# Kernel optimization log

Measured on AMD Instinct MI355X. Metric: run time of the kernel, lower is better.

## Reference

```python
import jax, jax.numpy as jnp
import numpy as np

N_NODES = 100000
N_EDGES = 1600000
IN_CH = 128
HID = 256
OUT_CH = 128
N_GRAPHS = 2048


def setup_inputs() -> dict:
    key = jax.random.key(0)
    ks = jax.random.split(key, 12)
    x = jax.random.normal(ks[0], (N_NODES, IN_CH), dtype=jnp.float32)
    edge_index = jax.random.randint(ks[1], (2, N_EDGES), 0, N_NODES, dtype=jnp.int32)
    batch = jnp.sort(jax.random.randint(ks[2], (N_NODES,), 0, N_GRAPHS, dtype=jnp.int32))
    s = lambda k, shp, fan: jax.random.normal(k, shp, dtype=jnp.float32) / np.sqrt(fan)
    params = {
        # SAGEConv1: lin_l (applied to aggregated neighbors, has bias) and lin_r (root)
        "W1l": s(ks[3], (IN_CH, HID), IN_CH), "b1": jnp.zeros((HID,), jnp.float32),
        "W1r": s(ks[4], (IN_CH, HID), IN_CH),
        # SAGEConv2
        "W2l": s(ks[5], (HID, HID), HID), "b2": jnp.zeros((HID,), jnp.float32),
        "W2r": s(ks[6], (HID, HID), HID),
        # MLP head
        "W3": s(ks[7], (HID, HID), HID), "b3": jnp.zeros((HID,), jnp.float32),
        "W4": s(ks[8], (HID, OUT_CH), HID), "b4": jnp.zeros((OUT_CH,), jnp.float32),
    }
    return {"x": x, "edge_index": edge_index, "batch": batch, **params}


def _sage_conv(x, src, dst, Wl, bl, Wr, num_nodes):
    # PyG SAGEConv (aggr='mean'): out_i = Wl @ mean_{j->i} x_j + bl + Wr @ x_i
    agg = jax.ops.segment_sum(x[src], dst, num_segments=num_nodes)  # [N, C]
    cnt = jax.ops.segment_sum(jnp.ones((src.shape[0],), x.dtype), dst, num_segments=num_nodes)
    mean = agg / jnp.maximum(cnt, 1.0)[:, None]
    return mean @ Wl + bl + x @ Wr


def reference(x, edge_index, batch, W1l, b1, W1r, W2l, b2, W2r, W3, b3, W4, b4):
    src, dst = edge_index[0], edge_index[1]
    h = jax.nn.relu(_sage_conv(x, src, dst, W1l, b1, W1r, N_NODES))
    # dropout is identity in eval mode
    h = jax.nn.relu(_sage_conv(h, src, dst, W2l, b2, W2r, N_NODES))
    # global_mean_pool over graphs
    psum = jax.ops.segment_sum(h, batch, num_segments=N_GRAPHS)  # [G, HID]
    gcnt = jax.ops.segment_sum(jnp.ones((h.shape[0],), h.dtype), batch, num_segments=N_GRAPHS)
    pooled = psum / jnp.maximum(gcnt, 1.0)[:, None]
    # MLP head
    hidden = jax.nn.relu(pooled @ W3 + b3)
    return hidden @ W4 + b4  # [G, OUT_CH]
```

## Files before the change

### kernel.cpp

```cpp
#include <hip/hip_runtime.h>

#define N_NODES 100000
#define N_EDGES 1600000
#define IN_CH 128
#define HID 256
#define OUT_CH 128
#define N_GRAPHS 2048

#define NBUK 391
#define CHUNK 8192

typedef __attribute__((ext_vector_type(8))) short bf16x8;
typedef __attribute__((ext_vector_type(4))) float f32x4;
typedef __attribute__((ext_vector_type(2))) float f32x2;

__device__ inline unsigned short f2b(float f) {
    unsigned int u = __builtin_bit_cast(unsigned int, f);
    u = (u + 0x7FFF + ((u >> 16) & 1)) >> 16;
    return (unsigned short)u;
}
__device__ inline float b2f(unsigned short h) {
    unsigned int u = (unsigned int)h << 16;
    return __builtin_bit_cast(float, u);
}

#define GLOAD_LDS16(gsrc, ldst)                                                   \
    __builtin_amdgcn_global_load_lds(                                             \
        (const __attribute__((address_space(1))) void*)(gsrc),                    \
        (__attribute__((address_space(3))) void*)(ldst), 16, 0, 0)

#define SCAN_ITEMS 8
#define SCAN_TILE (256 * SCAN_ITEMS)

__global__ void scan1_k(const int* __restrict__ in, int* __restrict__ out,
                        int* __restrict__ bsums, int n) {
    __shared__ int wsum[4];
    int base = blockIdx.x * SCAN_TILE + (int)threadIdx.x * SCAN_ITEMS;
    int v[SCAN_ITEMS];
    int s = 0;
    #pragma unroll
    for (int i = 0; i < SCAN_ITEMS; ++i) {
        v[i] = (base + i < n) ? in[base + i] : 0;
        s += v[i];
    }
    int lane = threadIdx.x & 63, wid = threadIdx.x >> 6;
    int incl = s;
    #pragma unroll
    for (int off = 1; off < 64; off <<= 1) {
        int t = __shfl_up(incl, off, 64);
        if (lane >= off) incl += t;
    }
    if (lane == 63) wsum[wid] = incl;
    __syncthreads();
    int wprefix = 0;
    #pragma unroll
    for (int w = 0; w < 4; ++w)
        if (w < wid) wprefix += wsum[w];
    int run = wprefix + incl - s;
    #pragma unroll
    for (int i = 0; i < SCAN_ITEMS; ++i) {
        if (base + i < n) out[base + i] = run;
        run += v[i];
    }
    if (threadIdx.x == 255) bsums[blockIdx.x] = wprefix + incl;
}

__global__ void scan2_k(int* __restrict__ bsums, int nb, int* __restrict__ total) {
    __shared__ int wsum[4];
    int v = ((int)threadIdx.x < nb) ? bsums[threadIdx.x] : 0;
    int lane = threadIdx.x & 63, wid = threadIdx.x >> 6;
    int incl = v;
    #pragma unroll
    for (int off = 1; off < 64; off <<= 1) {
        int t = __shfl_up(incl, off, 64);
        if (lane >= off) incl += t;
    }
    if (lane == 63) wsum[wid] = incl;
    __syncthreads();
    int wprefix = 0;
    #pragma unroll
    for (int w = 0; w < 4; ++w)
        if (w < wid) wprefix += wsum[w];
    if ((int)threadIdx.x < nb) bsums[threadIdx.x] = wprefix + incl - v;
    if (threadIdx.x == 255) *total = wprefix + incl;
}

__global__ void bucket_count_k(const int* __restrict__ dst, int* __restrict__ bcnt, int E) {
    __shared__ int cnt[NBUK];
    int tid = threadIdx.x;
    for (int i = tid; i < NBUK; i += 256) cnt[i] = 0;
    __syncthreads();
    int e0 = blockIdx.x * CHUNK;
    int eend = min(e0 + CHUNK, E);
    for (int e = e0 + tid; e < eend; e += 256)
        atomicAdd(&cnt[dst[e] >> 8], 1);
    __syncthreads();
    for (int i = tid; i < NBUK; i += 256)
        if (cnt[i]) atomicAdd(&bcnt[i], cnt[i]);
}

__global__ void bin_scatter_k(const int* __restrict__ src, const int* __restrict__ dst,
                              const int* __restrict__ bbase, int* __restrict__ bcur,
                              uint2* __restrict__ staging, int E) {
    __shared__ int cnt[NBUK];
    __shared__ int gbase[NBUK];
    int tid = threadIdx.x;
    for (int i = tid; i < NBUK; i += 256) cnt[i] = 0;
    __syncthreads();
    int e0 = blockIdx.x * CHUNK;
    int eend = min(e0 + CHUNK, E);
    for (int e = e0 + tid; e < eend; e += 256)
        atomicAdd(&cnt[dst[e] >> 8], 1);
    __syncthreads();
    for (int i = tid; i < NBUK; i += 256) {
        int c = cnt[i];
        gbase[i] = c ? (bbase[i] + atomicAdd(&bcur[i], c)) : 0;
        cnt[i] = 0;
    }
    __syncthreads();
    for (int e = e0 + tid; e < eend; e += 256) {
        int d = dst[e];
        int b = d >> 8;
        int l = atomicAdd(&cnt[b], 1);
        uint2 p; p.x = (unsigned)src[e]; p.y = (unsigned)d;
        staging[(size_t)gbase[b] + l] = p;
    }
}

__global__ void csr_build_k(const uint2* __restrict__ staging, const int* __restrict__ bbase,
                            int* __restrict__ row_ofs, int* __restrict__ csr) {
    __shared__ int ldeg[256];
    __shared__ int lofs[256];
    __shared__ int wsum[4];
    int b = blockIdx.x, tid = threadIdx.x;
    int base = bbase[b];
    int cnt = bbase[b + 1] - base;
    ldeg[tid] = 0;
    __syncthreads();
    const uint2* sp = staging + base;
    for (int i = tid; i < cnt; i += 256)
        atomicAdd(&ldeg[sp[i].y & 255], 1);
    __syncthreads();
    int v = ldeg[tid];
    int lane = tid & 63, wid = tid >> 6;
    int incl = v;
    #pragma unroll
    for (int off = 1; off < 64; off <<= 1) {
        int t = __shfl_up(incl, off, 64);
        if (lane >= off) incl += t;
    }
    if (lane == 63) wsum[wid] = incl;
    __syncthreads();
    int wprefix = 0;
    #pragma unroll
    for (int w = 0; w < 4; ++w)
        if (w < wid) wprefix += wsum[w];
    int excl = wprefix + incl - v;
    lofs[tid] = excl;
    int node = b * 256 + tid;
    if (node < N_NODES) row_ofs[node] = base + excl;
    if (b == NBUK - 1 && tid == 0) row_ofs[N_NODES] = N_EDGES;
    ldeg[tid] = 0;
    __syncthreads();
    for (int i = tid; i < cnt; i += 256) {
        uint2 p = sp[i];
        int d = (int)p.y & 255;
        int pos = atomicAdd(&ldeg[d], 1);
        csr[base + lofs[d] + pos] = (int)p.x;
    }
}

__global__ void gofs_search_k(const int* __restrict__ batch, int* __restrict__ gofs,
                              int n, int G) {
    int g = blockIdx.x * blockDim.x + threadIdx.x;
    if (g > G) return;
    if (g == G) { gofs[G] = n; return; }
    int lo = 0, hi = n;
    while (lo < hi) {
        int mid = (lo + hi) >> 1;
        if (batch[mid] < g) lo = mid + 1; else hi = mid;
    }
    gofs[g] = lo;
}

__global__ void wt_concat_k(const float* __restrict__ Wl, const float* __restrict__ Wr,
                            unsigned short* __restrict__ out, int K1, int K2, int N) {
    int idx = blockIdx.x * blockDim.x + threadIdx.x;
    int KT = K1 + K2;
    if (idx >= N * KT) return;
    int n = idx / KT, k = idx % KT;
    float v = (k < K1) ? Wl[(size_t)k * N + n] : Wr[(size_t)(k - K1) * N + n];
    out[idx] = f2b(v);
}

__global__ void f2b8_k(const float* __restrict__ in, unsigned short* __restrict__ outb,
                       unsigned char* __restrict__ out8, size_t n8) {
    size_t i = (size_t)blockIdx.x * blockDim.x + threadIdx.x;
    if (i >= n8) return;
    float4 a = ((const float4*)in)[i * 2];
    float4 b = ((const float4*)in)[i * 2 + 1];
    unsigned short ob[8];
    ob[0] = f2b(a.x); ob[1] = f2b(a.y); ob[2] = f2b(a.z); ob[3] = f2b(a.w);
    ob[4] = f2b(b.x); ob[5] = f2b(b.y); ob[6] = f2b(b.z); ob[7] = f2b(b.w);
    ((uint4*)outb)[i] = *(const uint4*)ob;
    int w0 = 0, w1 = 0;
    w0 = __builtin_amdgcn_cvt_pk_fp8_f32(a.x, a.y, w0, false);
    w0 = __builtin_amdgcn_cvt_pk_fp8_f32(a.z, a.w, w0, true);
    w1 = __builtin_amdgcn_cvt_pk_fp8_f32(b.x, b.y, w1, false);
    w1 = __builtin_amdgcn_cvt_pk_fp8_f32(b.z, b.w, w1, true);
    uint2 o8; o8.x = (unsigned int)w0; o8.y = (unsigned int)w1;
    ((uint2*)out8)[i] = o8;
}

__global__ void b2f8_k(const unsigned short* __restrict__ in, unsigned char* __restrict__ out,
                       size_t n16) {
    size_t i = (size_t)blockIdx.x * blockDim.x + threadIdx.x;
    if (i >= n16) return;
    uint4 v0 = ((const uint4*)in)[i * 2];
    uint4 v1 = ((const uint4*)in)[i * 2 + 1];
    const unsigned int* q = (const unsigned int*)&v0;
    const unsigned int* r = (const unsigned int*)&v1;
    uint4 o;
    unsigned int* po = (unsigned int*)&o;
    #pragma unroll
    for (int t = 0; t < 2; ++t) {
        int w = 0;
        w = __builtin_amdgcn_cvt_pk_fp8_f32(b2f((unsigned short)(q[t * 2] & 0xFFFF)),
                                            b2f((unsigned short)(q[t * 2] >> 16)), w, false);
        w = __builtin_amdgcn_cvt_pk_fp8_f32(b2f((unsigned short)(q[t * 2 + 1] & 0xFFFF)),
                                            b2f((unsigned short)(q[t * 2 + 1] >> 16)), w, true);
        po[t] = (unsigned int)w;
    }
    #pragma unroll
    for (int t = 0; t < 2; ++t) {
        int w = 0;
        w = __builtin_amdgcn_cvt_pk_fp8_f32(b2f((unsigned short)(r[t * 2] & 0xFFFF)),
                                            b2f((unsigned short)(r[t * 2] >> 16)), w, false);
        w = __builtin_amdgcn_cvt_pk_fp8_f32(b2f((unsigned short)(r[t * 2 + 1] & 0xFFFF)),
                                            b2f((unsigned short)(r[t * 2 + 1] >> 16)), w, true);
        po[2 + t] = (unsigned int)w;
    }
    ((uint4*)out)[i] = o;
}

template <int C>
__global__ void agg_f8_k(const unsigned char* __restrict__ X8, const int* __restrict__ row_ofs,
                         const int* __restrict__ csr, unsigned short* __restrict__ out, int n) {
    constexpr int GL = C / 16;
    constexpr int NG = 64 / GL;
    int w = (int)((blockIdx.x * blockDim.x + threadIdx.x) >> 6);
    int lane = threadIdx.x & 63;
    if (w >= n) return;
    int g = lane / GL, il = lane % GL;
    int s = row_ofs[w], e = row_ofs[w + 1];
    float a[16];
    #pragma unroll
    for (int t = 0; t < 16; ++t) a[t] = 0.f;

    int j = s + g;
    for (; j + NG < e; j += 2 * NG) {
        int i0 = csr[j], i1 = csr[j + NG];
        uint4 r0 = *(const uint4*)&X8[(size_t)i0 * C + il * 16];
        uint4 r1 = *(const uint4*)&X8[(size_t)i1 * C + il * 16];
        const unsigned int* q0 = (const unsigned int*)&r0;
        const unsigned int* q1 = (const unsigned int*)&r1;
        #pragma unroll
        for (int t = 0; t < 4; ++t) {
            f32x2 lo = __builtin_amdgcn_cvt_pk_f32_fp8(q0[t], false);
            f32x2 hi = __builtin_amdgcn_cvt_pk_f32_fp8(q0[t], true);
            a[t * 4 + 0] += lo.x; a[t * 4 + 1] += lo.y;
            a[t * 4 + 2] += hi.x; a[t * 4 + 3] += hi.y;
        }
        #pragma unroll
        for (int t = 0; t < 4; ++t) {
            f32x2 lo = __builtin_amdgcn_cvt_pk_f32_fp8(q1[t], false);
            f32x2 hi = __builtin_amdgcn_cvt_pk_f32_fp8(q1[t], true);
            a[t * 4 + 0] += lo.x; a[t * 4 + 1] += lo.y;
            a[t * 4 + 2] += hi.x; a[t * 4 + 3] += hi.y;
        }
    }
    if (j < e) {
        int i0 = csr[j];
        uint4 r0 = *(const uint4*)&X8[(size_t)i0 * C + il * 16];
        const unsigned int* q0 = (const unsigned int*)&r0;
        #pragma unroll
        for (int t = 0; t < 4; ++t) {
            f32x2 lo = __builtin_amdgcn_cvt_pk_f32_fp8(q0[t], false);
            f32x2 hi = __builtin_amdgcn_cvt_pk_f32_fp8(q0[t], true);
            a[t * 4 + 0] += lo.x; a[t * 4 + 1] += lo.y;
            a[t * 4 + 2] += hi.x; a[t * 4 + 3] += hi.y;
        }
    }

    #pragma unroll
    for (int m = GL; m < 64; m <<= 1)
        #pragma unroll
        for (int t = 0; t < 16; ++t) a[t] += __shfl_xor(a[t], m, 64);

    if (g == 0) {
        float inv = 1.0f / (float)max(e - s, 1);
        uint4 o0, o1;
        unsigned short* p0 = (unsigned short*)&o0;
        unsigned short* p1 = (unsigned short*)&o1;
        #pragma unroll
        for (int t = 0; t < 8; ++t) p0[t] = f2b(a[t] * inv);
        #pragma unroll
        for (int t = 0; t < 8; ++t) p1[t] = f2b(a[8 + t] * inv);
        *(uint4*)&out[(size_t)w * C + il * 16] = o0;
        *(uint4*)&out[(size_t)w * C + il * 16 + 8] = o1;
    }
}

__global__ void pool_mean_k(const unsigned short* __restrict__ H, const int* __restrict__ gofs,
                            float* __restrict__ pooled, int G) {
    int g = (int)((blockIdx.x * blockDim.x + threadIdx.x) >> 6);
    int lane = threadIdx.x & 63;
    if (g >= G) return;
    int s = gofs[g], e = gofs[g + 1];
    float a0 = 0.f, a1 = 0.f, a2 = 0.f, a3 = 0.f;
    for (int r = s; r < e; ++r) {
        ushort4 t = ((const ushort4*)(H + (size_t)r * HID))[lane];
        a0 += b2f(t.x); a1 += b2f(t.y); a2 += b2f(t.z); a3 += b2f(t.w);
    }
    float inv = 1.0f / (float)max(e - s, 1);
    float4 o; o.x = a0 * inv; o.y = a1 * inv; o.z = a2 * inv; o.w = a3 * inv;
    ((float4*)(pooled + (size_t)g * HID))[lane] = o;
}

__launch_bounds__(256)
__global__ void mfma_gemm_k(const unsigned short* __restrict__ A1, int K1,
                            const unsigned short* __restrict__ A2, int K2,
                            const unsigned short* __restrict__ Bt,
                            const float* __restrict__ bias, int M, int Nfull,
                            void* __restrict__ Cptr, int c_bf16, int do_relu) {
    __shared__ short ldsA[2 * 128 * 32];
    __shared__ short ldsB[2 * 128 * 32];
    int tid = threadIdx.x, lane = tid & 63;
    int wid = tid >> 6, wm = wid >> 1, wn = wid & 1;
    int row0 = blockIdx.x * 128, col0 = blockIdx.y * 128;
    int q = lane >> 4, l15 = lane & 15;
    int KT = K1 + K2;
    int nk = KT / 32;

    int rr = tid >> 2;
    int c8 = (tid & 3) * 8;
    int dof = wid * 512;

    auto stage = [&](int t) {
        int kt = t * 32;
        const unsigned short* Asrc; int kk, Ks;
        if (kt < K1) { Asrc = A1; kk = kt; Ks = K1; }
        else         { Asrc = A2; kk = kt - K1; Ks = K2; }
        short* bA = ldsA + (t & 1) * 4096;
        short* bB = ldsB + (t & 1) * 4096;
        #pragma unroll
        for (int h = 0; h < 2; ++h) {
            int r = h * 64 + rr;
            int gr = min(row0 + r, M - 1);
            GLOAD_LDS16(Asrc + (size_t)gr * Ks + kk + c8, bA + h * 2048 + dof);
            GLOAD_LDS16(Bt + (size_t)(col0 + r) * KT + kt + c8, bB + h * 2048 + dof);
        }
    };

    f32x4 acc[4][4] = {};

    stage(0);
    stage(1);

    for (int t = 0; t < nk; ++t) {
        if (t == nk - 1) asm volatile("s_waitcnt vmcnt(0)" ::: "memory");
        else             asm volatile("s_waitcnt vmcnt(4)" ::: "memory");
        asm volatile("s_barrier" ::: "memory");

        const short* bA = ldsA + (t & 1) * 4096;
        const short* bB = ldsB + (t & 1) * 4096;
        bf16x8 af[4], bfr[4];
        #pragma unroll
        for (int i = 0; i < 4; ++i)
            af[i] = *(const bf16x8*)&bA[(wm * 64 + i * 16 + l15) * 32 + q * 8];
        #pragma unroll
        for (int j = 0; j < 4; ++j)
            bfr[j] = *(const bf16x8*)&bB[(wn * 64 + j * 16 + l15) * 32 + q * 8];
        #pragma unroll
        for (int i = 0; i < 4; ++i)
            #pragma unroll
            for (int j = 0; j < 4; ++j)
                acc[i][j] = __builtin_amdgcn_mfma_f32_16x16x32_bf16(af[i], bfr[j], acc[i][j], 0, 0, 0);

        asm volatile("s_barrier" ::: "memory");
        if (t + 2 < nk) stage(t + 2);
    }

    #pragma unroll
    for (int i = 0; i < 4; ++i) {
        #pragma unroll
        for (int reg = 0; reg < 4; ++reg) {
            int r = row0 + wm * 64 + i * 16 + q * 4 + reg;
            if (r < M) {
                #pragma unroll
                for (int j = 0; j < 4; ++j) {
                    int cc = col0 + wn * 64 + j * 16 + l15;
                    float v = acc[i][j][reg] + bias[cc];
                    if (do_relu) v = fmaxf(v, 0.f);
                    if (c_bf16) ((unsigned short*)Cptr)[(size_t)r * Nfull + cc] = f2b(v);
                    else        ((float*)Cptr)[(size_t)r * Nfull + cc] = v;
                }
            }
        }
    }
}

#define BM_ 64
#define BK_ 16

template <int BN_>
__launch_bounds__(256)
__global__ void gemm2_k(const float* __restrict__ A1, const float* __restrict__ B1, int K1,
                        const float* __restrict__ bias, float* __restrict__ C,
                        int M, int N, int do_relu) {
    constexpr int TCOLS = BN_ / 8;
    constexpr int TROWS = 256 / TCOLS;
    constexpr int TM = BM_ / TROWS;
    __shared__ float As[BK_][BM_ + 4];
    __shared__ float Bs[BK_][BN_ + 4];
    int tid = threadIdx.x;
    int row0 = blockIdx.x * BM_;
    int col0 = blockIdx.y * BN_;
    int tx = tid % TCOLS, ty = tid / TCOLS;

    float acc[TM][8];
    #pragma unroll
    for (int i = 0; i < TM; ++i)
        #pragma unroll
        for (int j = 0; j < 8; ++j) acc[i][j] = 0.f;

    int ar = tid >> 2;
    int ak = (tid & 3) * 4;

    for (int kt = 0; kt < K1; kt += BK_) {
        {
            int r = row0 + ar;
            int rc = min(r, M - 1);
            float4 v = *(const float4*)(A1 + (size_t)rc * K1 + kt + ak);
            As[ak + 0][ar] = v.x;
            As[ak + 1][ar] = v.y;
            As[ak + 2][ar] = v.z;
            As[ak + 3][ar] = v.w;
        }
        {
            #pragma unroll
            for (int h = 0; h < BN_ / 64; ++h) {
                int idx = h * 256 + tid;
                int kr = idx / (BN_ / 4);
                int c4 = idx % (BN_ / 4);
                float4 v = *(const float4*)(B1 + (size_t)(kt + kr) * N + col0 + c4 * 4);
                *(float4*)&Bs[kr][c4 * 4] = v;
            }
        }
        __syncthreads();

        #pragma unroll
        for (int k = 0; k < BK_; ++k) {
            float a[TM], b[8];
            #pragma unroll
            for (int v = 0; v < TM / 4; ++v)
                *(float4*)&a[v * 4] = *(const float4*)&As[k][ty * TM + v * 4];
            *(float4*)&b[0] = *(const float4*)&Bs[k][tx * 8];
            *(float4*)&b[4] = *(const float4*)&Bs[k][tx * 8 + 4];
            #pragma unroll
            for (int i = 0; i < TM; ++i)
                #pragma unroll
                for (int j = 0; j < 8; ++j) acc[i][j] = fmaf(a[i], b[j], acc[i][j]);
        }
        __syncthreads();
    }

    float bv[8];
    #pragma unroll
    for (int j = 0; j < 8; ++j) bv[j] = bias[col0 + tx * 8 + j];
    #pragma unroll
    for (int i = 0; i < TM; ++i) {
        int r = row0 + ty * TM + i;
        if (r < M) {
            float* cp = C + (size_t)r * N + col0 + tx * 8;
            float o[8];
            #pragma unroll
            for (int j = 0; j < 8; ++j) {
                float v = acc[i][j] + bv[j];
                o[j] = do_relu ? fmaxf(v, 0.f) : v;
            }
            *(float4*)(cp + 0) = *(float4*)&o[0];
            *(float4*)(cp + 4) = *(float4*)&o[4];
        }
    }
}

extern "C" void kernel_launch(void* const* d_in, const int* in_sizes, int n_in,
                              void* d_out, int out_size, void* d_ws, size_t ws_size,
                              hipStream_t stream) {
    const float* x    = (const float*)d_in[0];
    const int*   ei   = (const int*)d_in[1];
    const int*   batch= (const int*)d_in[2];
    const float* W1l  = (const float*)d_in[3];
    const float* b1   = (const float*)d_in[4];
    const float* W1r  = (const float*)d_in[5];
    const float* W2l  = (const float*)d_in[6];
    const float* b2   = (const float*)d_in[7];
    const float* W2r  = (const float*)d_in[8];
    const float* W3   = (const float*)d_in[9];
    const float* b3   = (const float*)d_in[10];
    const float* W4   = (const float*)d_in[11];
    const float* b4   = (const float*)d_in[12];
    float* out = (float*)d_out;

    const int N = N_NODES, E = N_EDGES, G = N_GRAPHS;
    const int* src = ei;
    const int* dst = ei + E;

    char* ws = (char*)d_ws;
    size_t off = 0;
    auto alloc = [&](size_t bytes) -> char* {
        off = (off + 255) & ~(size_t)255;
        char* p = ws + off;
        off += bytes;
        return p;
    };
    int* bcnt    = (int*)alloc((size_t)NBUK * 4);
    int* bcur    = (int*)alloc((size_t)NBUK * 4);
    size_t zero_span = (size_t)((char*)(bcur + NBUK) - (char*)bcnt);
    int* bbase   = (int*)alloc((size_t)(NBUK + 1) * 4);
    int* bsums   = (int*)alloc(256 * 4);
    int* row_ofs = (int*)alloc((size_t)(N + 1) * 4);
    int* gofs    = (int*)alloc((size_t)(G + 1) * 4);
    uint2* staging = (uint2*)alloc((size_t)E * 8);
    int* csr     = (int*)alloc((size_t)E * 4);
    unsigned short* xb    = (unsigned short*)alloc((size_t)N * IN_CH * 2);
    unsigned short* mean1 = (unsigned short*)alloc((size_t)N * IN_CH * 2);
    unsigned short* h1    = (unsigned short*)alloc((size_t)N * HID * 2);
    unsigned short* mean2 = (unsigned short*)alloc((size_t)N * HID * 2);
    unsigned short* h2    = xb;
    unsigned char*  x8    = (unsigned char*)alloc((size_t)N * IN_CH);
    unsigned char*  h1f8  = (unsigned char*)alloc((size_t)N * HID);
    unsigned short* W1T   = (unsigned short*)alloc((size_t)HID * (IN_CH + IN_CH) * 2);
    unsigned short* W2T   = (unsigned short*)alloc((size_t)HID * (HID + HID) * 2);
    float* pooled = (float*)alloc((size_t)G * HID * 4);
    float* hidden = (float*)alloc((size_t)G * HID * 4);
    (void)ws_size;

    hipMemsetAsync(bcnt, 0, zero_span, stream);

    const int EB = (E + CHUNK - 1) / CHUNK;
    bucket_count_k<<<EB, 256, 0, stream>>>(dst, bcnt, E);
    scan1_k<<<1, 256, 0, stream>>>(bcnt, bbase, bsums, NBUK);
    scan2_k<<<1, 256, 0, stream>>>(bsums, 1, bbase + NBUK);
    bin_scatter_k<<<EB, 256, 0, stream>>>(src, dst, bbase, bcur, staging, E);
    csr_build_k<<<NBUK, 256, 0, stream>>>(staging, bbase, row_ofs, csr);

    gofs_search_k<<<(G + 256) / 256, 256, 0, stream>>>(batch, gofs, N, G);

    wt_concat_k<<<(HID * 2 * IN_CH + 255) / 256, 256, 0, stream>>>(W1l, W1r, W1T, IN_CH, IN_CH, HID);
    wt_concat_k<<<(HID * 2 * HID + 255) / 256, 256, 0, stream>>>(W2l, W2r, W2T, HID, HID, HID);
    f2b8_k<<<(int)(((size_t)N * IN_CH / 8 + 255) / 256), 256, 0, stream>>>(
        x, xb, x8, (size_t)N * IN_CH / 8);

    const int MB = (N + 127) / 128;

    agg_f8_k<IN_CH><<<(N + 3) / 4, 256, 0, stream>>>(x8, row_ofs, csr, mean1, N);
    mfma_gemm_k<<<dim3(MB, HID / 128), 256, 0, stream>>>(
        mean1, IN_CH, xb, IN_CH, W1T, b1, N, HID, h1, 1, 1);

    b2f8_k<<<(int)(((size_t)N * HID / 16 + 255) / 256), 256, 0, stream>>>(
        h1, h1f8, (size_t)N * HID / 16);

    agg_f8_k<HID><<<(N + 3) / 4, 256, 0, stream>>>(h1f8, row_ofs, csr, mean2, N);
    mfma_gemm_k<<<dim3(MB, HID / 128), 256, 0, stream>>>(
        mean2, HID, h1, HID, W2T, b2, N, HID, h2, 1, 1);

    pool_mean_k<<<(G + 3) / 4, 256, 0, stream>>>(h2, gofs, pooled, G);

    gemm2_k<HID><<<dim3(G / BM_, 1), 256, 0, stream>>>(
        pooled, W3, HID, b3, hidden, G, HID, 1);
    gemm2_k<OUT_CH><<<dim3(G / BM_, 1), 256, 0, stream>>>(
        hidden, W4, HID, b4, out, G, OUT_CH, 0);
}
```

Baseline: 560.4 us.

## Triple-buffer GEMM LDS stages and remap layout to k-chunk-major

The bf16 MFMA GEMM moves from two to three LDS buffers and prefetches three k-tiles ahead, with the vmcnt waits adjusted, so more global-load latency is hidden. The LDS tile layout also changes: each wave now loads one 8-element k-chunk for 64 rows, stored k-chunk-major, and fragment reads index accordingly. This is meant to remove LDS bank conflicts on the 16-byte fragment reads. In exchange LDS use per block rises, which may lower occupancy, and the global loads become less coalesced (16 bytes per row per lane instead of 64 contiguous bytes).

```diff
diff --git a/kernel.cpp b/kernel.cpp
--- a/kernel.cpp
+++ b/kernel.cpp
@@ -333,8 +333,8 @@
                             const unsigned short* __restrict__ Bt,
                             const float* __restrict__ bias, int M, int Nfull,
                             void* __restrict__ Cptr, int c_bf16, int do_relu) {
-    __shared__ short ldsA[2 * 128 * 32];
-    __shared__ short ldsB[2 * 128 * 32];
+    __shared__ short ldsA[3 * 4096];
+    __shared__ short ldsB[3 * 4096];
     int tid = threadIdx.x, lane = tid & 63;
     int wid = tid >> 6, wm = wid >> 1, wn = wid & 1;
     int row0 = blockIdx.x * 128, col0 = blockIdx.y * 128;
@@ -342,23 +342,20 @@
     int KT = K1 + K2;
     int nk = KT / 32;
 
-    int rr = tid >> 2;
-    int c8 = (tid & 3) * 8;
-    int dof = wid * 512;
-
     auto stage = [&](int t) {
         int kt = t * 32;
         const unsigned short* Asrc; int kk, Ks;
         if (kt < K1) { Asrc = A1; kk = kt; Ks = K1; }
         else         { Asrc = A2; kk = kt - K1; Ks = K2; }
-        short* bA = ldsA + (t & 1) * 4096;
-        short* bB = ldsB + (t & 1) * 4096;
+        int buf = t % 3;
+        short* bA = ldsA + buf * 4096;
+        short* bB = ldsB + buf * 4096;
         #pragma unroll
         for (int h = 0; h < 2; ++h) {
-            int r = h * 64 + rr;
+            int r = h * 64 + lane;
             int gr = min(row0 + r, M - 1);
-            GLOAD_LDS16(Asrc + (size_t)gr * Ks + kk + c8, bA + h * 2048 + dof);
-            GLOAD_LDS16(Bt + (size_t)(col0 + r) * KT + kt + c8, bB + h * 2048 + dof);
+            GLOAD_LDS16(Asrc + (size_t)gr * Ks + kk + wid * 8, bA + h * 2048 + wid * 512);
+            GLOAD_LDS16(Bt + (size_t)(col0 + r) * KT + kt + wid * 8, bB + h * 2048 + wid * 512);
         }
     };
 
@@ -366,21 +363,24 @@
 
     stage(0);
     stage(1);
+    stage(2);
 
     for (int t = 0; t < nk; ++t) {
-        if (t == nk - 1) asm volatile("s_waitcnt vmcnt(0)" ::: "memory");
-        else             asm volatile("s_waitcnt vmcnt(4)" ::: "memory");
+        if (t < nk - 2)       asm volatile("s_waitcnt vmcnt(8)" ::: "memory");
+        else if (t == nk - 2) asm volatile("s_waitcnt vmcnt(4)" ::: "memory");
+        else                  asm volatile("s_waitcnt vmcnt(0)" ::: "memory");
         asm volatile("s_barrier" ::: "memory");
 
-        const short* bA = ldsA + (t & 1) * 4096;
-        const short* bB = ldsB + (t & 1) * 4096;
+        int buf = t % 3;
+        const short* bA = ldsA + buf * 4096;
+        const short* bB = ldsB + buf * 4096;
         bf16x8 af[4], bfr[4];
         #pragma unroll
         for (int i = 0; i < 4; ++i)
-            af[i] = *(const bf16x8*)&bA[(wm * 64 + i * 16 + l15) * 32 + q * 8];
+            af[i] = *(const bf16x8*)&bA[wm * 2048 + q * 512 + (i * 16 + l15) * 8];
         #pragma unroll
         for (int j = 0; j < 4; ++j)
-            bfr[j] = *(const bf16x8*)&bB[(wn * 64 + j * 16 + l15) * 32 + q * 8];
+            bfr[j] = *(const bf16x8*)&bB[wn * 2048 + q * 512 + (j * 16 + l15) * 8];
         #pragma unroll
         for (int i = 0; i < 4; ++i)
             #pragma unroll
@@ -388,7 +388,7 @@
                 acc[i][j] = __builtin_amdgcn_mfma_f32_16x16x32_bf16(af[i], bfr[j], acc[i][j], 0, 0, 0);
 
         asm volatile("s_barrier" ::: "memory");
-        if (t + 2 < nk) stage(t + 2);
+        if (t + 3 < nk) stage(t + 3);
     }
 
     #pragma unroll
```

New measurement: 589.2 us. 5.1% more time.
